# Optimization experiments

Measured on AMD Instinct MI355X. Metric: run time of the kernel, lower is better.

## Reference

```python
import jax, jax.numpy as jnp
import numpy as np
from jax import lax

B, C = 16, 1024          # batch, in_channels (= spectral length)
N_HEAD = 8
N_FEAT = 512
CH = N_FEAT // N_HEAD    # 64 per-head channels
EPS = 1e-5


def setup_inputs() -> dict:
    key = jax.random.key(0)
    ks = jax.random.split(key, 9)
    x = jax.random.normal(ks[0], (B, C), dtype=jnp.float32)
    # BatchNorm1d (inference mode) params / running stats
    bn_gamma = jax.random.normal(ks[1], (C,), dtype=jnp.float32) * 0.1 + 1.0
    bn_beta = jax.random.normal(ks[2], (C,), dtype=jnp.float32) * 0.1
    bn_mean = jax.random.normal(ks[3], (C,), dtype=jnp.float32) * 0.1
    bn_var = jax.random.uniform(ks[4], (C,), dtype=jnp.float32, minval=0.5, maxval=1.5)
    # in_conv: Conv1d(1, 3*N_FEAT, kernel=3, stride=1, pad=1) -> weight [O, I, K]
    w_in = jax.random.normal(ks[5], (3 * N_FEAT, 1, 3), dtype=jnp.float32) * (1.0 / np.sqrt(3))
    b_in = jax.random.normal(ks[6], (3 * N_FEAT,), dtype=jnp.float32) * 0.02
    # proj_h: Conv1d(N_FEAT, 1, kernel=1). zero_module zeros it at init; use
    # nonzero values so the reference exercises the full graph (trained state).
    w_out = jax.random.normal(ks[7], (1, N_FEAT, 1), dtype=jnp.float32) * (1.0 / np.sqrt(N_FEAT))
    b_out = jax.random.normal(ks[8], (1,), dtype=jnp.float32) * 0.02
    return {"x": x, "bn_gamma": bn_gamma, "bn_beta": bn_beta, "bn_mean": bn_mean,
            "bn_var": bn_var, "w_in": w_in, "b_in": b_in, "w_out": w_out, "b_out": b_out}


def reference(x, bn_gamma, bn_beta, bn_mean, bn_var, w_in, b_in, w_out, b_out):
    b, c = x.shape
    # BatchNorm1d on [b, c] input (eval mode, per-channel stats)
    xn = (x - bn_mean) * jax.lax.rsqrt(bn_var + EPS) * bn_gamma + bn_beta
    x1 = xn[:, None, :]  # [b, 1, c]
    # Conv1d(1 -> 3*N_FEAT, k=3, pad=1)
    qkv = lax.conv_general_dilated(
        x1, w_in, window_strides=(1,), padding=((1, 1),),
        dimension_numbers=("NCH", "OIH", "NCH")) + b_in[None, :, None]  # [b, 3F, c]
    # QKVAttentionLegacy: reshape to [b*H, 3*ch, c], split, scaled dot-product
    qkv = qkv.reshape(b * N_HEAD, 3 * CH, c)
    q, k, v = jnp.split(qkv, 3, axis=1)          # each [b*H, ch, c]
    scale = CH ** -0.25
    w = jnp.einsum("bct,bcs->bts", q * scale, k * scale)  # [b*H, c, c]
    w = jax.nn.softmax(w, axis=-1)
    a = jnp.einsum("bts,bcs->bct", w, v)          # [b*H, ch, c]
    h = a.reshape(b, N_FEAT, c)
    # proj_h: 1x1 conv N_FEAT -> 1
    h = jnp.einsum("of,bft->bot", w_out[:, :, 0][None].squeeze(0)[None].squeeze(0)[None] if False else w_out[:, :, 0], h) + b_out[None, :, None]  # [b, 1, c]
    return (h + x1).reshape(b, c)
```

## Files before the change

kernel.cpp:

```cpp
#include <hip/hip_runtime.h>
#include <hip/hip_bf16.h>
#include <math.h>

#define NB 16
#define SEQ 1024
#define NHEAD 8
#define NBH (NB*NHEAD)

typedef __attribute__((ext_vector_type(4))) float f32x4;

#define OFF_XN 0u
#define OFF_VP 65536u
#define OFF_M  (65536u + 524288u)

__device__ __forceinline__ void load_lds16(const void* g, void* l) {
  __builtin_amdgcn_global_load_lds(
      (const __attribute__((address_space(1))) void*)g,
      (__attribute__((address_space(3))) void*)l, 16, 0, 0);
}

__global__ void __launch_bounds__(256) k_prep(
    const float* __restrict__ x, const float* __restrict__ gam,
    const float* __restrict__ be, const float* __restrict__ mu,
    const float* __restrict__ va, const float* __restrict__ w_in,
    const float* __restrict__ b_in, const float* __restrict__ w_out,
    const float* __restrict__ b_out,
    float* __restrict__ xng, float* __restrict__ vpg,
    float* __restrict__ Mws, float* __restrict__ out) {
  __shared__ float xsl[1025];
  __shared__ float hcs[4];
  int bid = blockIdx.x;
  int b = bid >> 3, h = bid & 7;
  int tid = threadIdx.x;
  int t4 = tid * 4;

  f32x4 xv = *(const f32x4*)(x + b*SEQ + t4);
  f32x4 muv = *(const f32x4*)(mu + t4);
  f32x4 vav = *(const f32x4*)(va + t4);
  f32x4 gv  = *(const f32x4*)(gam + t4);
  f32x4 bev = *(const f32x4*)(be + t4);
  f32x4 xn4;
  #pragma unroll
  for (int u = 0; u < 4; ++u)
    xn4[u] = (xv[u] - muv[u]) * rsqrtf(vav[u] + 1e-5f) * gv[u] + bev[u];
  *(f32x4*)(xsl + t4) = xn4;
  if (tid == 0) xsl[1024] = 0.f;
  if (h == 0) {
    *(f32x4*)(xng + b*SEQ + t4) = xn4;
    float bo = b_out[0];
    f32x4 o4 = {xn4[0]+bo, xn4[1]+bo, xn4[2]+bo, xn4[3]+bo};
    *(f32x4*)(out + b*SEQ + t4) = o4;
  }

  {
    int j = tid >> 6, c = tid & 63;
    int o = h*192 + 128 + c;
    float wv = (j < 3) ? w_in[o*3 + j] : b_in[o];
    float p = w_out[h*64 + c] * wv;
    #pragma unroll
    for (int mk = 1; mk < 64; mk <<= 1) p += __shfl_xor(p, mk);
    if (c == 0) hcs[j] = p;
  }

  {
    int ij = tid >> 4, cq = tid & 15;
    int i = ij >> 2, j = ij & 3;
    float acc = 0.f;
    #pragma unroll
    for (int u = 0; u < 4; ++u) {
      int c = cq*4 + u;
      int oq = h*192 + c, ok = oq + 64;
      float wq = (i < 3) ? w_in[oq*3 + i] : b_in[oq];
      float wk = (j < 3) ? w_in[ok*3 + j] : b_in[ok];
      acc = fmaf(wq, wk, acc);
    }
    #pragma unroll
    for (int mk = 1; mk < 16; mk <<= 1) acc += __shfl_xor(acc, mk);
    if (cq == 0) Mws[h*16 + ij] = acc * (0.125f * 1.4426950408889634f);
  }
  __syncthreads();

  float hc0 = hcs[0], hc1 = hcs[1], hc2 = hcs[2], hc3 = hcs[3];
  f32x4 vp4;
  #pragma unroll
  for (int u = 0; u < 4; ++u) {
    int t = t4 + u;
    float xm = (t > 0) ? xsl[t-1] : 0.f;
    float xp = xsl[t+1];
    vp4[u] = fmaf(hc0, xm, fmaf(hc1, xsl[t], fmaf(hc2, xp, hc3)));
  }
  *(f32x4*)(vpg + (b*NHEAD + h)*SEQ + t4) = vp4;
}

__global__ void __launch_bounds__(256) k_attn(
    const float* __restrict__ xng, const float* __restrict__ vpg,
    const float* __restrict__ Mws, float* __restrict__ out) {
  __shared__ float xsl[1032];
  __shared__ float vps[1032];
  __shared__ float Ms[16];
  int bid = blockIdx.x;
  int bh = bid & 127, chunk = bid >> 7;
  int b = bh >> 3, h = bh & 7;
  int tid = threadIdx.x;

  load_lds16((const char*)(xng + b*SEQ)  + tid*16, (char*)xsl + tid*16);
  load_lds16((const char*)(vpg + bh*SEQ) + tid*16, (char*)vps + tid*16);
  if (tid < 8) { xsl[1024+tid] = 0.f; vps[1024+tid] = 0.f; }
  if (tid < 16) Ms[tid] = Mws[h*16 + tid];
  __syncthreads();

  int t = chunk*256 + tid;
  float um = (t > 0) ? xsl[t-1] : 0.f;
  float u0 = xsl[t], up = xsl[t+1];
  float a0 = fmaf(um, Ms[0], fmaf(u0, Ms[4],  fmaf(up, Ms[8],  Ms[12])));
  float a1 = fmaf(um, Ms[1], fmaf(u0, Ms[5],  fmaf(up, Ms[9],  Ms[13])));
  float a2 = fmaf(um, Ms[2], fmaf(u0, Ms[6],  fmaf(up, Ms[10], Ms[14])));
  float a3 = fmaf(um, Ms[3], fmaf(u0, Ms[7],  fmaf(up, Ms[11], Ms[15])));

  const f32x4* x4 = (const f32x4*)xsl;
  const f32x4* v4 = (const f32x4*)vps;
  float ss = 0.f, dd = 0.f;
  f32x4 cA = x4[0], vA = v4[0];
  f32x4 cB = x4[1], vB = v4[1];
  float prevW = 0.f;

#define STEP(XM, X0, XP, VV) { \
  float sc = fmaf(a0, (XM), fmaf(a1, (X0), fmaf(a2, (XP), a3))); \
  float p = __builtin_amdgcn_exp2f(sc); \
  ss += p; dd = fmaf(p, (VV), dd); }

  #pragma unroll 4
  for (int k = 0; k < 256; ++k) {
    f32x4 cC = x4[k+2];
    f32x4 vC = v4[k+2];
    STEP(prevW, cA.x, cA.y, vA.x)
    STEP(cA.x,  cA.y, cA.z, vA.y)
    STEP(cA.y,  cA.z, cA.w, vA.z)
    STEP(cA.z,  cA.w, cB.x, vA.w)
    prevW = cA.w; cA = cB; cB = cC; vA = vB; vB = vC;
  }
#undef STEP

  atomicAdd(&out[b*SEQ + t], dd / ss);
}

extern "C" void kernel_launch(void* const* d_in, const int* in_sizes, int n_in,
                              void* d_out, int out_size, void* d_ws, size_t ws_size,
                              hipStream_t stream) {
  const float* x   = (const float*)d_in[0];
  const float* g   = (const float*)d_in[1];
  const float* be  = (const float*)d_in[2];
  const float* mu  = (const float*)d_in[3];
  const float* va  = (const float*)d_in[4];
  const float* win = (const float*)d_in[5];
  const float* bin = (const float*)d_in[6];
  const float* wo  = (const float*)d_in[7];
  const float* bo  = (const float*)d_in[8];
  float* out = (float*)d_out;

  char* ws = (char*)d_ws;
  float* xng = (float*)(ws + OFF_XN);
  float* vpg = (float*)(ws + OFF_VP);
  float* Mws = (float*)(ws + OFF_M);

  hipLaunchKernelGGL(k_prep, dim3(NBH), dim3(256), 0, stream,
                     x, g, be, mu, va, win, bin, wo, bo, xng, vpg, Mws, out);
  hipLaunchKernelGGL(k_attn, dim3(NBH * 4), dim3(256), 0, stream,
                     xng, vpg, Mws, out);
}
```

Measured before the change: 97.66 us.

## Fuse prep and attention kernels into one per-batch-chunk kernel without atomics

```diff
diff --git a/kernel.cpp b/kernel.cpp
--- a/kernel.cpp
+++ b/kernel.cpp
@@ -1,40 +1,30 @@
 #include <hip/hip_runtime.h>
-#include <hip/hip_bf16.h>
 #include <math.h>
 
 #define NB 16
 #define SEQ 1024
 #define NHEAD 8
-#define NBH (NB*NHEAD)
 
 typedef __attribute__((ext_vector_type(4))) float f32x4;
 
-#define OFF_XN 0u
-#define OFF_VP 65536u
-#define OFF_M  (65536u + 524288u)
-
-__device__ __forceinline__ void load_lds16(const void* g, void* l) {
-  __builtin_amdgcn_global_load_lds(
-      (const __attribute__((address_space(1))) void*)g,
-      (__attribute__((address_space(3))) void*)l, 16, 0, 0);
-}
-
-__global__ void __launch_bounds__(256) k_prep(
+__global__ void __launch_bounds__(256) k_fused(
     const float* __restrict__ x, const float* __restrict__ gam,
     const float* __restrict__ be, const float* __restrict__ mu,
     const float* __restrict__ va, const float* __restrict__ w_in,
     const float* __restrict__ b_in, const float* __restrict__ w_out,
-    const float* __restrict__ b_out,
-    float* __restrict__ xng, float* __restrict__ vpg,
-    float* __restrict__ Mws, float* __restrict__ out) {
-  __shared__ float xsl[1025];
-  __shared__ float hcs[4];
+    const float* __restrict__ b_out, float* __restrict__ out) {
+  __shared__ float xsl[1032];
+  __shared__ float vps[NHEAD][1032];
+  __shared__ float Ms[NHEAD][16];
+  __shared__ float hcs[NHEAD][4];
+  __shared__ float rsum[NHEAD][32];
+
   int bid = blockIdx.x;
-  int b = bid >> 3, h = bid & 7;
+  int b = bid >> 5, chunk = bid & 31;
   int tid = threadIdx.x;
+
   int t4 = tid * 4;
-
-  f32x4 xv = *(const f32x4*)(x + b*SEQ + t4);
+  f32x4 xv  = *(const f32x4*)(x + b*SEQ + t4);
   f32x4 muv = *(const f32x4*)(mu + t4);
   f32x4 vav = *(const f32x4*)(va + t4);
   f32x4 gv  = *(const f32x4*)(gam + t4);
@@ -44,81 +34,57 @@
   for (int u = 0; u < 4; ++u)
     xn4[u] = (xv[u] - muv[u]) * rsqrtf(vav[u] + 1e-5f) * gv[u] + bev[u];
   *(f32x4*)(xsl + t4) = xn4;
-  if (tid == 0) xsl[1024] = 0.f;
-  if (h == 0) {
-    *(f32x4*)(xng + b*SEQ + t4) = xn4;
-    float bo = b_out[0];
-    f32x4 o4 = {xn4[0]+bo, xn4[1]+bo, xn4[2]+bo, xn4[3]+bo};
-    *(f32x4*)(out + b*SEQ + t4) = o4;
-  }
+  if (tid < 8) xsl[1024 + tid] = 0.f;
 
-  {
-    int j = tid >> 6, c = tid & 63;
-    int o = h*192 + 128 + c;
-    float wv = (j < 3) ? w_in[o*3 + j] : b_in[o];
-    float p = w_out[h*64 + c] * wv;
-    #pragma unroll
-    for (int mk = 1; mk < 64; mk <<= 1) p += __shfl_xor(p, mk);
-    if (c == 0) hcs[j] = p;
-  }
-
-  {
-    int ij = tid >> 4, cq = tid & 15;
-    int i = ij >> 2, j = ij & 3;
+  const float QS2 = 0.125f * 1.4426950408889634f;
+  if (tid < 128) {
+    int hh = tid >> 4, ij = tid & 15, i = ij >> 2, j = ij & 3;
+    int oq = hh * 192, ok = oq + 64;
     float acc = 0.f;
-    #pragma unroll
-    for (int u = 0; u < 4; ++u) {
-      int c = cq*4 + u;
-      int oq = h*192 + c, ok = oq + 64;
-      float wq = (i < 3) ? w_in[oq*3 + i] : b_in[oq];
-      float wk = (j < 3) ? w_in[ok*3 + j] : b_in[ok];
+    #pragma unroll 8
+    for (int c = 0; c < 64; ++c) {
+      float wq = (i < 3) ? w_in[(oq + c)*3 + i] : b_in[oq + c];
+      float wk = (j < 3) ? w_in[(ok + c)*3 + j] : b_in[ok + c];
       acc = fmaf(wq, wk, acc);
     }
-    #pragma unroll
-    for (int mk = 1; mk < 16; mk <<= 1) acc += __shfl_xor(acc, mk);
-    if (cq == 0) Mws[h*16 + ij] = acc * (0.125f * 1.4426950408889634f);
+    Ms[hh][ij] = acc * QS2;
+  } else if (tid < 160) {
+    int idx = tid - 128, hh = idx >> 2, jj = idx & 3;
+    int ov = hh * 192 + 128;
+    float acc = 0.f;
+    #pragma unroll 8
+    for (int c = 0; c < 64; ++c) {
+      float wv = (jj < 3) ? w_in[(ov + c)*3 + jj] : b_in[ov + c];
+      acc = fmaf(w_out[hh*64 + c], wv, acc);
+    }
+    hcs[hh][jj] = acc;
   }
   __syncthreads();
 
-  float hc0 = hcs[0], hc1 = hcs[1], hc2 = hcs[2], hc3 = hcs[3];
-  f32x4 vp4;
-  #pragma unroll
-  for (int u = 0; u < 4; ++u) {
-    int t = t4 + u;
-    float xm = (t > 0) ? xsl[t-1] : 0.f;
-    float xp = xsl[t+1];
-    vp4[u] = fmaf(hc0, xm, fmaf(hc1, xsl[t], fmaf(hc2, xp, hc3)));
+  int h = tid >> 5, tl = tid & 31;
+  {
+    float hc0 = hcs[h][0], hc1 = hcs[h][1], hc2 = hcs[h][2], hc3 = hcs[h][3];
+    #pragma unroll 4
+    for (int k2 = 0; k2 < 32; ++k2) {
+      int s = k2*32 + tl;
+      float xm = (s > 0) ? xsl[s-1] : 0.f;
+      vps[h][s] = fmaf(hc0, xm, fmaf(hc1, xsl[s], fmaf(hc2, xsl[s+1], hc3)));
+    }
+    if (tl < 8) vps[h][1024 + tl] = 0.f;
   }
-  *(f32x4*)(vpg + (b*NHEAD + h)*SEQ + t4) = vp4;
-}
-
-__global__ void __launch_bounds__(256) k_attn(
-    const float* __restrict__ xng, const float* __restrict__ vpg,
-    const float* __restrict__ Mws, float* __restrict__ out) {
-  __shared__ float xsl[1032];
-  __shared__ float vps[1032];
-  __shared__ float Ms[16];
-  int bid = blockIdx.x;
-  int bh = bid & 127, chunk = bid >> 7;
-  int b = bh >> 3, h = bh & 7;
-  int tid = threadIdx.x;
-
-  load_lds16((const char*)(xng + b*SEQ)  + tid*16, (char*)xsl + tid*16);
-  load_lds16((const char*)(vpg + bh*SEQ) + tid*16, (char*)vps + tid*16);
-  if (tid < 8) { xsl[1024+tid] = 0.f; vps[1024+tid] = 0.f; }
-  if (tid < 16) Ms[tid] = Mws[h*16 + tid];
   __syncthreads();
 
-  int t = chunk*256 + tid;
+  int t = chunk*32 + tl;
   float um = (t > 0) ? xsl[t-1] : 0.f;
   float u0 = xsl[t], up = xsl[t+1];
-  float a0 = fmaf(um, Ms[0], fmaf(u0, Ms[4],  fmaf(up, Ms[8],  Ms[12])));
-  float a1 = fmaf(um, Ms[1], fmaf(u0, Ms[5],  fmaf(up, Ms[9],  Ms[13])));
-  float a2 = fmaf(um, Ms[2], fmaf(u0, Ms[6],  fmaf(up, Ms[10], Ms[14])));
-  float a3 = fmaf(um, Ms[3], fmaf(u0, Ms[7],  fmaf(up, Ms[11], Ms[15])));
+  const float* Mh = Ms[h];
+  float a0 = fmaf(um, Mh[0], fmaf(u0, Mh[4],  fmaf(up, Mh[8],  Mh[12])));
+  float a1 = fmaf(um, Mh[1], fmaf(u0, Mh[5],  fmaf(up, Mh[9],  Mh[13])));
+  float a2 = fmaf(um, Mh[2], fmaf(u0, Mh[6],  fmaf(up, Mh[10], Mh[14])));
+  float a3 = fmaf(um, Mh[3], fmaf(u0, Mh[7],  fmaf(up, Mh[11], Mh[15])));
 
   const f32x4* x4 = (const f32x4*)xsl;
-  const f32x4* v4 = (const f32x4*)vps;
+  const f32x4* v4 = (const f32x4*)&vps[h][0];
   float ss = 0.f, dd = 0.f;
   f32x4 cA = x4[0], vA = v4[0];
   f32x4 cB = x4[1], vB = v4[1];
@@ -141,7 +107,16 @@
   }
 #undef STEP
 
-  atomicAdd(&out[b*SEQ + t], dd / ss);
+  rsum[h][tl] = dd / ss;
+  __syncthreads();
+
+  if (tid < 32) {
+    int to = chunk*32 + tid;
+    float acc = xsl[to] + b_out[0];
+    #pragma unroll
+    for (int hh = 0; hh < NHEAD; ++hh) acc += rsum[hh][tid];
+    out[b*SEQ + to] = acc;
+  }
 }
 
 extern "C" void kernel_launch(void* const* d_in, const int* in_sizes, int n_in,
@@ -157,14 +132,8 @@
   const float* wo  = (const float*)d_in[7];
   const float* bo  = (const float*)d_in[8];
   float* out = (float*)d_out;
+  (void)d_ws; (void)ws_size; (void)in_sizes; (void)n_in; (void)out_size;
 
-  char* ws = (char*)d_ws;
-  float* xng = (float*)(ws + OFF_XN);
-  float* vpg = (float*)(ws + OFF_VP);
-  float* Mws = (float*)(ws + OFF_M);
-
-  hipLaunchKernelGGL(k_prep, dim3(NBH), dim3(256), 0, stream,
-                     x, g, be, mu, va, win, bin, wo, bo, xng, vpg, Mws, out);
-  hipLaunchKernelGGL(k_attn, dim3(NBH * 4), dim3(256), 0, stream,
-                     xng, vpg, Mws, out);
+  hipLaunchKernelGGL(k_fused, dim3(NB * 32), dim3(256), 0, stream,
+                     x, g, be, mu, va, win, bin, wo, bo, out);
 }
```

Result: slower. 102.7 us (+5.2%).
